# Kernel optimization log

Hardware: AMD Instinct MI355X
Metric: run time of the kernel (lower is better)

## Reference

```python
import jax, jax.numpy as jnp
import numpy as np

EMBED = 768
HEADS = 12
D_K = EMBED // HEADS  # 64


def setup_inputs() -> dict:
    key = jax.random.key(0)
    ks = jax.random.split(key, 9)
    w_scale = EMBED ** -0.5
    inp = {
        "x": jax.random.normal(ks[0], (128, 256, 1, EMBED), dtype=jnp.float32),
        "Wq": jax.random.normal(ks[1], (EMBED, EMBED), dtype=jnp.float32) * w_scale,
        "bq": jax.random.normal(ks[2], (EMBED,), dtype=jnp.float32) * 0.02,
        "Wk": jax.random.normal(ks[3], (EMBED, EMBED), dtype=jnp.float32) * w_scale,
        "bk": jax.random.normal(ks[4], (EMBED,), dtype=jnp.float32) * 0.02,
        "Wv": jax.random.normal(ks[5], (EMBED, EMBED), dtype=jnp.float32) * w_scale,
        "bv": jax.random.normal(ks[6], (EMBED,), dtype=jnp.float32) * 0.02,
        "Wo": jax.random.normal(ks[7], (EMBED, EMBED), dtype=jnp.float32) * w_scale,
        "bo": jax.random.normal(ks[8], (EMBED,), dtype=jnp.float32) * 0.02,
    }
    return inp


def reference(x, Wq, bq, Wk, bk, Wv, bv, Wo, bo):
    # x: (n_rows r, n_cols i/j, batch n, embed)
    R, C, B, E = x.shape
    H, Dk = HEADS, D_K
    # tied-row scaling: d_k^{-1/2} / sqrt(n_rows)
    scaling = (Dk ** -0.5) / np.sqrt(R).astype(np.float32)

    q = (x @ Wq.T + bq).reshape(R, C, B, H, Dk) * scaling
    k = (x @ Wk.T + bk).reshape(R, C, B, H, Dk)
    v = (x @ Wv.T + bv).reshape(R, C, B, H, Dk)

    # scores summed over rows r and head dim d -> (h, n, i, j)
    scores = jnp.einsum('rinhd,rjnhd->hnij', q, k)
    probs = jax.nn.softmax(scores, axis=-1)  # dropout p=0 -> identity

    # shared attention applied per row
    c = jnp.einsum('hnij,rjnhd->rinhd', probs, v).reshape(R, C, B, E)
    out = c @ Wo.T + bo
    return (out, probs)
```

## Files before the change

kernel.cpp:

```cpp
#include <hip/hip_runtime.h>
#include <math.h>

typedef short bf16x8 __attribute__((ext_vector_type(8)));
typedef float f32x4 __attribute__((ext_vector_type(4)));
typedef unsigned short ushort8 __attribute__((ext_vector_type(8)));
typedef unsigned short ushort4v __attribute__((ext_vector_type(4)));

constexpr int R = 128, Cc = 256, E = 768, H = 12;
constexpr int M = R * Cc;
constexpr size_t TOK = (size_t)M * E;

__device__ __forceinline__ unsigned short f2b(float f) {
  unsigned int u = __float_as_uint(f);
  u += 0x7fff + ((u >> 16) & 1);
  return (unsigned short)(u >> 16);
}

__device__ __forceinline__ void ldst16(const unsigned short* g, unsigned short* l) {
  __builtin_amdgcn_global_load_lds(
      (const __attribute__((address_space(1))) unsigned int*)g,
      (__attribute__((address_space(3))) unsigned int*)l, 16, 0, 0);
}

__global__ __launch_bounds__(256) void cvt_bf16(const float* __restrict__ in,
                                                unsigned short* __restrict__ out,
                                                int n8) {
  int i = blockIdx.x * 256 + threadIdx.x;
  if (i >= n8) return;
  const float4* p = (const float4*)in;
  float4 a = p[2 * i], b = p[2 * i + 1];
  ushort8 o;
  o[0] = f2b(a.x); o[1] = f2b(a.y); o[2] = f2b(a.z); o[3] = f2b(a.w);
  o[4] = f2b(b.x); o[5] = f2b(b.y); o[6] = f2b(b.z); o[7] = f2b(b.w);
  ((ushort8*)out)[i] = o;
}

__device__ __forceinline__ void stage64(const unsigned short* __restrict__ A, int lda,
                                        const unsigned short* __restrict__ B, int ldb,
                                        int k0, unsigned short* As, unsigned short* Bs,
                                        int wv, int ln, int srow, int scol) {
#pragma unroll
  for (int t = 0; t < 4; ++t) {
    const int ch = wv * 4 + t;
    const int row = ch * 8 + srow;
    ldst16(A + (size_t)row * lda + k0 + scol, As + ch * 512 + ln * 8);
    ldst16(B + (size_t)row * ldb + k0 + scol, Bs + ch * 512 + ln * 8);
  }
}

__device__ __forceinline__ void gemm128(const unsigned short* __restrict__ A, int lda,
                                        const unsigned short* __restrict__ B, int ldb,
                                        int K, unsigned short* As, unsigned short* Bs,
                                        int wv, int ln, int wm, int wn,
                                        f32x4 (&acc)[4][4]) {
  const int srow = ln >> 3;
  const int scol = ((ln & 7) ^ srow) * 8;
  const int nt = K >> 6;
  stage64(A, lda, B, ldb, 0, As, Bs, wv, ln, srow, scol);
  if (nt > 1)
    stage64(A, lda, B, ldb, 64, As + 8192, Bs + 8192, wv, ln, srow, scol);
  for (int t = 0; t < nt; ++t) {
    const int cur = t & 1;
    if (t + 1 < nt) {
      asm volatile("s_waitcnt vmcnt(8)" ::: "memory");
    } else {
      asm volatile("s_waitcnt vmcnt(0)" ::: "memory");
    }
    __builtin_amdgcn_sched_barrier(0);
    __builtin_amdgcn_s_barrier();
    const unsigned short* Ab = As + cur * 8192;
    const unsigned short* Bb = Bs + cur * 8192;
    bf16x8 a[2][4], b[2][4];
#pragma unroll
    for (int dk = 0; dk < 2; ++dk) {
      const int rc = ((dk * 4 + (ln >> 4)) ^ (ln & 7)) * 8;
#pragma unroll
      for (int i = 0; i < 4; ++i)
        a[dk][i] = *(const bf16x8*)(Ab + (wm + i * 16 + (ln & 15)) * 64 + rc);
#pragma unroll
      for (int j = 0; j < 4; ++j)
        b[dk][j] = *(const bf16x8*)(Bb + (wn + j * 16 + (ln & 15)) * 64 + rc);
    }
    asm volatile("s_waitcnt lgkmcnt(0)" ::: "memory");
    __builtin_amdgcn_sched_barrier(0);
    __builtin_amdgcn_s_barrier();
    if (t + 2 < nt)
      stage64(A, lda, B, ldb, (t + 2) * 64, As + cur * 8192, Bs + cur * 8192,
              wv, ln, srow, scol);
#pragma unroll
    for (int dk = 0; dk < 2; ++dk)
#pragma unroll
      for (int i = 0; i < 4; ++i)
#pragma unroll
        for (int j = 0; j < 4; ++j)
          acc[i][j] = __builtin_amdgcn_mfma_f32_16x16x32_bf16(a[dk][i], b[dk][j],
                                                              acc[i][j], 0, 0, 0);
  }
}

__global__ __launch_bounds__(256) void qkv_proj(
    const unsigned short* __restrict__ A, const unsigned short* __restrict__ B,
    const float* __restrict__ bq, const float* __restrict__ bk,
    const float* __restrict__ bv, unsigned short* __restrict__ q2,
    unsigned short* __restrict__ k2, unsigned short* __restrict__ v3, float scaling) {
  __shared__ unsigned short As[2 * 128 * 64];
  __shared__ unsigned short Bs[2 * 128 * 64];
  const int tid = threadIdx.x, wv = tid >> 6, ln = tid & 63;
  const unsigned p = blockIdx.x + blockIdx.y * 18;
  const unsigned l = (p & 7) * 576 + (p >> 3);
  const int bx = l % 18, by = l / 18;
  const int n0 = bx * 128, m0 = by * 128;
  const int wm = (wv & 1) * 64, wn = (wv >> 1) * 64;
  f32x4 acc[4][4] = {};
  gemm128(A + (size_t)m0 * 768, 768, B + (size_t)n0 * 768, 768, 768,
          As, Bs, wv, ln, wm, wn, acc);

  const int region = bx / 6;
  const float* bias = region == 0 ? bq : (region == 1 ? bk : bv);
  const float sc = region == 0 ? scaling : 1.0f;
  const int nq0 = n0 - region * 768;
#pragma unroll
  for (int j = 0; j < 4; ++j) {
    const int np = nq0 + wn + j * 16 + (ln & 15);
    const int h = np >> 6, d = np & 63;
    const float bn = bias[np];
#pragma unroll
    for (int i = 0; i < 4; ++i) {
      const int mb = m0 + wm + i * 16 + (ln >> 4) * 4;
      if (region < 2) {
        unsigned short* dst = region == 0 ? q2 : k2;
#pragma unroll
        for (int r = 0; r < 4; ++r) {
          const int m = mb + r;
          const int ic = m & 255, rr = m >> 8;
          dst[(size_t)h * 2097152 + (size_t)ic * 8192 + rr * 64 + d] =
              f2b((acc[i][j][r] + bn) * sc);
        }
      } else {
        const int jc = mb & 255, rr = mb >> 8;
        ushort4v o;
#pragma unroll
        for (int r = 0; r < 4; ++r) o[r] = f2b(acc[i][j][r] + bn);
        *(ushort4v*)(v3 + (size_t)h * 2097152 + ((size_t)rr * 64 + d) * 256 + jc) = o;
      }
    }
  }
}

__global__ __launch_bounds__(256) void qk_gemm(const unsigned short* __restrict__ q2,
                                               const unsigned short* __restrict__ k2,
                                               float* __restrict__ Sp) {
  __shared__ unsigned short As[2 * 128 * 64];
  __shared__ unsigned short Bs[2 * 128 * 64];
  const int tid = threadIdx.x, wv = tid >> 6, ln = tid & 63;
  const int i0 = (blockIdx.x & 1) * 128, j0 = (blockIdx.x >> 1) * 128;
  const int h = blockIdx.y, kc = blockIdx.z;
  const int wm = (wv & 1) * 64, wn = (wv >> 1) * 64;
  f32x4 acc[4][4] = {};
  const unsigned short* Ap = q2 + (size_t)h * 2097152 + (size_t)i0 * 8192 + kc * 1024;
  const unsigned short* Bp = k2 + (size_t)h * 2097152 + (size_t)j0 * 8192 + kc * 1024;
  gemm128(Ap, 8192, Bp, 8192, 1024, As, Bs, wv, ln, wm, wn, acc);
  float* out = Sp + ((size_t)kc * H + h) * 65536;
#pragma unroll
  for (int j = 0; j < 4; ++j) {
    const int jj = j0 + wn + j * 16 + (ln & 15);
#pragma unroll
    for (int i = 0; i < 4; ++i)
#pragma unroll
      for (int r = 0; r < 4; ++r) {
        const int ii = i0 + wm + i * 16 + (ln >> 4) * 4 + r;
        out[(size_t)ii * 256 + jj] = acc[i][j][r];
      }
  }
}

__global__ __launch_bounds__(256) void softmax_k(const float* __restrict__ Sp,
                                                 float* __restrict__ P,
                                                 unsigned short* __restrict__ Pb) {
  const int row = blockIdx.x, j = threadIdx.x;
  const size_t stride = (size_t)H * Cc * Cc;
  const size_t base = (size_t)row * Cc + j;
  float s = 0.f;
#pragma unroll
  for (int c = 0; c < 8; ++c) s += Sp[base + c * stride];
  float m = s;
#pragma unroll
  for (int o = 32; o > 0; o >>= 1) m = fmaxf(m, __shfl_xor(m, o));
  __shared__ float sm[4], ss[4];
  const int wid = j >> 6, lane = j & 63;
  if (lane == 0) sm[wid] = m;
  __syncthreads();
  m = fmaxf(fmaxf(sm[0], sm[1]), fmaxf(sm[2], sm[3]));
  float e = expf(s - m);
  float t = e;
#pragma unroll
  for (int o = 32; o > 0; o >>= 1) t += __shfl_xor(t, o);
  if (lane == 0) ss[wid] = t;
  __syncthreads();
  t = ss[0] + ss[1] + ss[2] + ss[3];
  const float p = e / t;
  P[base] = p;
  Pb[base] = f2b(p);
}

__global__ __launch_bounds__(256) void pv_gemm(const unsigned short* __restrict__ P,
                                               const unsigned short* __restrict__ V,
                                               unsigned short* __restrict__ Co) {
  __shared__ unsigned short As[2 * 128 * 64];
  __shared__ unsigned short Bs[2 * 128 * 64];
  const int tid = threadIdx.x, wv = tid >> 6, ln = tid & 63;
  const unsigned p = blockIdx.x + blockIdx.y * 128;
  const unsigned l = (p & 7) * 192 + (p >> 3);
  const int bx = l & 127, h = l >> 7;
  const int i0 = (bx & 1) * 128, n0 = (bx >> 1) * 128;
  const int wm = (wv & 1) * 64, wn = (wv >> 1) * 64;
  f32x4 acc[4][4] = {};
  const unsigned short* Ap = P + (size_t)h * 65536 + (size_t)i0 * 256;
  const unsigned short* Bp = V + (size_t)h * 2097152 + (size_t)n0 * 256;
  gemm128(Ap, 256, Bp, 256, 256, As, Bs, wv, ln, wm, wn, acc);
#pragma unroll
  for (int j = 0; j < 4; ++j) {
    const int n = n0 + wn + j * 16 + (ln & 15);
    const int rr = n >> 6, d = n & 63;
#pragma unroll
    for (int i = 0; i < 4; ++i)
#pragma unroll
      for (int r = 0; r < 4; ++r) {
        const int ii = i0 + wm + i * 16 + (ln >> 4) * 4 + r;
        Co[((size_t)rr * 256 + ii) * 768 + h * 64 + d] = f2b(acc[i][j][r]);
      }
  }
}

__global__ __launch_bounds__(256) void o_proj(const unsigned short* __restrict__ A,
                                              const unsigned short* __restrict__ B,
                                              const float* __restrict__ bias,
                                              float* __restrict__ Y) {
  __shared__ unsigned short As[2 * 128 * 64];
  __shared__ unsigned short Bs[2 * 128 * 64];
  const int tid = threadIdx.x, wv = tid >> 6, ln = tid & 63;
  const unsigned p = blockIdx.x + blockIdx.y * 6;
  const unsigned l = (p & 7) * 192 + (p >> 3);
  const int bx = l % 6, by = l / 6;
  const int n0 = bx * 128, m0 = by * 128;
  const int wm = (wv & 1) * 64, wn = (wv >> 1) * 64;
  f32x4 acc[4][4] = {};
  gemm128(A + (size_t)m0 * 768, 768, B + (size_t)n0 * 768, 768, 768,
          As, Bs, wv, ln, wm, wn, acc);
#pragma unroll
  for (int j = 0; j < 4; ++j) {
    const int n = n0 + wn + j * 16 + (ln & 15);
    const float bn = bias[n];
#pragma unroll
    for (int i = 0; i < 4; ++i)
#pragma unroll
      for (int r = 0; r < 4; ++r) {
        const int m = m0 + wm + i * 16 + (ln >> 4) * 4 + r;
        Y[(size_t)m * 768 + n] = acc[i][j][r] + bn;
      }
  }
}

extern "C" void kernel_launch(void* const* d_in, const int* in_sizes, int n_in,
                              void* d_out, int out_size, void* d_ws, size_t ws_size,
                              hipStream_t stream) {
  const float* x  = (const float*)d_in[0];
  const float* Wq = (const float*)d_in[1];
  const float* bq = (const float*)d_in[2];
  const float* Wk = (const float*)d_in[3];
  const float* bk = (const float*)d_in[4];
  const float* Wv = (const float*)d_in[5];
  const float* bv = (const float*)d_in[6];
  const float* Wo = (const float*)d_in[7];
  const float* bo = (const float*)d_in[8];
  float* out = (float*)d_out;
  float* probs = out + TOK;

  char* ws = (char*)d_ws;
  unsigned short* x_bf  = (unsigned short*)(ws);
  unsigned short* q2    = (unsigned short*)(ws + 50331648);
  unsigned short* k2    = (unsigned short*)(ws + 100663296);
  unsigned short* v3    = (unsigned short*)(ws + 150994944);
  unsigned short* Wq_bf = (unsigned short*)(ws + 201326592);
  unsigned short* Wk_bf = Wq_bf + 589824;
  unsigned short* Wv_bf = Wk_bf + 589824;
  unsigned short* Wo_bf = Wv_bf + 589824;
  float* S_part         = (float*)(ws);
  unsigned short* P_bf  = (unsigned short*)(ws + 25165824);
  unsigned short* c_bf  = q2;

  const float scaling = 0.125f / sqrtf(128.f);

  cvt_bf16<<<12288, 256, 0, stream>>>(x, x_bf, 3145728);
  cvt_bf16<<<288, 256, 0, stream>>>(Wq, Wq_bf, 73728);
  cvt_bf16<<<288, 256, 0, stream>>>(Wk, Wk_bf, 73728);
  cvt_bf16<<<288, 256, 0, stream>>>(Wv, Wv_bf, 73728);
  cvt_bf16<<<288, 256, 0, stream>>>(Wo, Wo_bf, 73728);

  qkv_proj<<<dim3(18, 256), 256, 0, stream>>>(x_bf, Wq_bf, bq, bk, bv,
                                              q2, k2, v3, scaling);

  qk_gemm<<<dim3(4, H, 8), 256, 0, stream>>>(q2, k2, S_part);
  softmax_k<<<H * Cc, 256, 0, stream>>>(S_part, probs, P_bf);
  pv_gemm<<<dim3(128, H), 256, 0, stream>>>(P_bf, v3, c_bf);

  o_proj<<<dim3(6, 256), 256, 0, stream>>>(c_bf, Wo_bf, bo, out);
}
```

Measured before the change: 492.1 us.

## Split GEMM LDS fragment loads and overlap first-half MFMAs; fuse weight conversions

The gemm128 inner loop now loads the two k-halves of the LDS fragments separately. It waits only for the first half (lgkmcnt(8)) and issues those MFMAs before the barrier and the next global-to-LDS stage, so LDS reads overlap with matrix math. MFMA sections are wrapped in s_setprio to favour the compute wave. The four separate weight bf16 conversion launches are also merged into one kernel to cut launch overhead. The main risks are extra register pressure and the schedule depending on exact waitcnt counts.

New measurement: 505.0 us. 2.6% more time.

```diff
diff --git a/kernel.cpp b/kernel.cpp
--- a/kernel.cpp
+++ b/kernel.cpp
@@ -33,6 +33,23 @@
   o[0] = f2b(a.x); o[1] = f2b(a.y); o[2] = f2b(a.z); o[3] = f2b(a.w);
   o[4] = f2b(b.x); o[5] = f2b(b.y); o[6] = f2b(b.z); o[7] = f2b(b.w);
   ((ushort8*)out)[i] = o;
+}
+
+__global__ __launch_bounds__(256) void cvt_w4(const float* __restrict__ W0,
+                                              const float* __restrict__ W1,
+                                              const float* __restrict__ W2,
+                                              const float* __restrict__ W3,
+                                              unsigned short* __restrict__ out) {
+  const int region = blockIdx.x / 288;
+  const int i = (blockIdx.x % 288) * 256 + threadIdx.x;
+  if (i >= 73728) return;
+  const float* src = region == 0 ? W0 : (region == 1 ? W1 : (region == 2 ? W2 : W3));
+  const float4* p = (const float4*)src;
+  float4 a = p[2 * i], b = p[2 * i + 1];
+  ushort8 o;
+  o[0] = f2b(a.x); o[1] = f2b(a.y); o[2] = f2b(a.z); o[3] = f2b(a.w);
+  o[4] = f2b(b.x); o[5] = f2b(b.y); o[6] = f2b(b.z); o[7] = f2b(b.w);
+  ((ushort8*)(out + (size_t)region * 589824))[i] = o;
 }
 
 __device__ __forceinline__ void stage64(const unsigned short* __restrict__ A, int lda,
@@ -71,30 +88,49 @@
     const unsigned short* Ab = As + cur * 8192;
     const unsigned short* Bb = Bs + cur * 8192;
     bf16x8 a[2][4], b[2][4];
-#pragma unroll
-    for (int dk = 0; dk < 2; ++dk) {
-      const int rc = ((dk * 4 + (ln >> 4)) ^ (ln & 7)) * 8;
+    {
+      const int rc0 = (((ln >> 4)) ^ (ln & 7)) * 8;
 #pragma unroll
       for (int i = 0; i < 4; ++i)
-        a[dk][i] = *(const bf16x8*)(Ab + (wm + i * 16 + (ln & 15)) * 64 + rc);
+        a[0][i] = *(const bf16x8*)(Ab + (wm + i * 16 + (ln & 15)) * 64 + rc0);
 #pragma unroll
       for (int j = 0; j < 4; ++j)
-        b[dk][j] = *(const bf16x8*)(Bb + (wn + j * 16 + (ln & 15)) * 64 + rc);
+        b[0][j] = *(const bf16x8*)(Bb + (wn + j * 16 + (ln & 15)) * 64 + rc0);
     }
+    __builtin_amdgcn_sched_barrier(0);
+    {
+      const int rc1 = ((4 + (ln >> 4)) ^ (ln & 7)) * 8;
+#pragma unroll
+      for (int i = 0; i < 4; ++i)
+        a[1][i] = *(const bf16x8*)(Ab + (wm + i * 16 + (ln & 15)) * 64 + rc1);
+#pragma unroll
+      for (int j = 0; j < 4; ++j)
+        b[1][j] = *(const bf16x8*)(Bb + (wn + j * 16 + (ln & 15)) * 64 + rc1);
+    }
+    asm volatile("s_waitcnt lgkmcnt(8)" ::: "memory");
+    __builtin_amdgcn_sched_barrier(0);
+    __builtin_amdgcn_s_setprio(1);
+#pragma unroll
+    for (int i = 0; i < 4; ++i)
+#pragma unroll
+      for (int j = 0; j < 4; ++j)
+        acc[i][j] = __builtin_amdgcn_mfma_f32_16x16x32_bf16(a[0][i], b[0][j],
+                                                            acc[i][j], 0, 0, 0);
+    __builtin_amdgcn_s_setprio(0);
     asm volatile("s_waitcnt lgkmcnt(0)" ::: "memory");
     __builtin_amdgcn_sched_barrier(0);
     __builtin_amdgcn_s_barrier();
     if (t + 2 < nt)
       stage64(A, lda, B, ldb, (t + 2) * 64, As + cur * 8192, Bs + cur * 8192,
               wv, ln, srow, scol);
-#pragma unroll
-    for (int dk = 0; dk < 2; ++dk)
-#pragma unroll
-      for (int i = 0; i < 4; ++i)
-#pragma unroll
-        for (int j = 0; j < 4; ++j)
-          acc[i][j] = __builtin_amdgcn_mfma_f32_16x16x32_bf16(a[dk][i], b[dk][j],
-                                                              acc[i][j], 0, 0, 0);
+    __builtin_amdgcn_s_setprio(1);
+#pragma unroll
+    for (int i = 0; i < 4; ++i)
+#pragma unroll
+      for (int j = 0; j < 4; ++j)
+        acc[i][j] = __builtin_amdgcn_mfma_f32_16x16x32_bf16(a[1][i], b[1][j],
+                                                            acc[i][j], 0, 0, 0);
+    __builtin_amdgcn_s_setprio(0);
   }
 }
 
@@ -292,10 +328,7 @@
   const float scaling = 0.125f / sqrtf(128.f);
 
   cvt_bf16<<<12288, 256, 0, stream>>>(x, x_bf, 3145728);
-  cvt_bf16<<<288, 256, 0, stream>>>(Wq, Wq_bf, 73728);
-  cvt_bf16<<<288, 256, 0, stream>>>(Wk, Wk_bf, 73728);
-  cvt_bf16<<<288, 256, 0, stream>>>(Wv, Wv_bf, 73728);
-  cvt_bf16<<<288, 256, 0, stream>>>(Wo, Wo_bf, 73728);
+  cvt_w4<<<1152, 256, 0, stream>>>(Wq, Wk, Wv, Wo, Wq_bf);
 
   qkv_proj<<<dim3(18, 256), 256, 0, stream>>>(x_bf, Wq_bf, bq, bk, bv,
                                               q2, k2, v3, scaling);
```
